# Optimization experiments

Measured on AMD Instinct MI355X. Metric: run time of the kernel, lower is better.

The kernel has to match this reference:

```python
import jax, jax.numpy as jnp
import numpy as np

B, N, IN_DIM, OUT_DIM, C = 8, 8192, 1024, 512, 64
TEMPERATURE = 1.0
LN_EPS = 1e-5


def setup_inputs() -> dict:
    key = jax.random.key(0)
    ks = jax.random.split(key, 6)
    node_embeddings = jax.random.normal(ks[0], (B, N, IN_DIM), dtype=jnp.float32)
    node_mask = jnp.zeros((B, N), dtype=bool)  # True => node is masked out
    # xavier_uniform for cluster_centers [C, OUT_DIM]
    lim_c = float(np.sqrt(6.0 / (C + OUT_DIM)))
    cluster_centers = jax.random.uniform(ks[1], (C, OUT_DIM), jnp.float32, -lim_c, lim_c)
    # nn.Linear default init (kaiming-uniform-ish bounds)
    lim_n = float(1.0 / np.sqrt(IN_DIM))
    W_node = jax.random.uniform(ks[2], (IN_DIM, OUT_DIM), jnp.float32, -lim_n, lim_n)
    b_node = jax.random.uniform(ks[3], (OUT_DIM,), jnp.float32, -lim_n, lim_n)
    lim_k = float(1.0 / np.sqrt(OUT_DIM))
    W_cluster = jax.random.uniform(ks[4], (OUT_DIM, OUT_DIM), jnp.float32, -lim_k, lim_k)
    b_cluster = jax.random.uniform(ks[5], (OUT_DIM,), jnp.float32, -lim_k, lim_k)
    ln_gamma = jnp.ones((OUT_DIM,), jnp.float32)
    ln_beta = jnp.zeros((OUT_DIM,), jnp.float32)
    return {
        "node_embeddings": node_embeddings,
        "node_mask": node_mask,
        "cluster_centers": cluster_centers,
        "W_node": W_node,
        "b_node": b_node,
        "W_cluster": W_cluster,
        "b_cluster": b_cluster,
        "ln_gamma": ln_gamma,
        "ln_beta": ln_beta,
    }


def reference(node_embeddings, node_mask, cluster_centers, W_node, b_node,
              W_cluster, b_cluster, ln_gamma, ln_beta):
    # node projection: [B, N, D]
    node_proj = jnp.einsum('bni,io->bno', node_embeddings, W_node) + b_node
    # projected cluster centers (batch-independent): [C, D]
    ccp = cluster_centers @ W_cluster + b_cluster
    # similarities: [B, C, N]
    sims = jnp.einsum('cd,bnd->bcn', ccp, node_proj) / TEMPERATURE
    sims = jnp.where(node_mask[:, None, :], -jnp.inf, sims)
    assignment_weights = jax.nn.softmax(sims, axis=-1)  # dropout is identity in eval
    # aggregate: [B, C, D], residual add of projected centers
    compressed = jnp.einsum('bcn,bnd->bcd', assignment_weights, node_proj) + ccp
    # LayerNorm over last dim
    mu = jnp.mean(compressed, axis=-1, keepdims=True)
    var = jnp.var(compressed, axis=-1, keepdims=True)
    compressed = (compressed - mu) * jax.lax.rsqrt(var + LN_EPS) * ln_gamma + ln_beta
    return compressed, assignment_weights
```

## Files before the change

### kernel.cpp

```cpp
#include <hip/hip_runtime.h>
#include <hip/hip_bf16.h>
#include <math.h>

#define Bn 8
#define Nn 8192
#define KIN 1024
#define DOUT 512
#define NC 64
#define LN_EPS 1e-5f

typedef short bf16x8 __attribute__((ext_vector_type(8)));
typedef short s8v __attribute__((ext_vector_type(8)));
typedef float f32x4 __attribute__((ext_vector_type(4)));

__device__ __forceinline__ short f2bf(float f) {
    __hip_bfloat16 h = __float2bfloat16(f);
    return __builtin_bit_cast(short, h);
}

__device__ __forceinline__ void load_lds16(const void* g, void* l) {
    __builtin_amdgcn_global_load_lds(
        (const __attribute__((address_space(1))) unsigned int*)g,
        (__attribute__((address_space(3))) unsigned int*)l, 16, 0, 0);
}

__global__ void k_prep_w(const float* __restrict__ W, short* __restrict__ Wt) {
    int o = blockIdx.x * 256 + threadIdx.x;
    int n = o >> 10, k = o & 1023;
    Wt[o] = f2bf(W[k * DOUT + n]);
}

__global__ void k_prep_c(const float* __restrict__ cc, const float* __restrict__ Wc,
                         const float* __restrict__ bc, float* __restrict__ ccp_f,
                         short* __restrict__ ccp_bf) {
    int o = blockIdx.x * 256 + threadIdx.x;
    int c = o >> 9, n = o & 511;
    float a = bc[n];
    for (int k = 0; k < DOUT; ++k) a += cc[c * DOUT + k] * Wc[k * DOUT + n];
    ccp_f[o] = a;
    ccp_bf[o] = f2bf(a);
}

__global__ __launch_bounds__(256) void k_gemm1(
    const float* __restrict__ A, const short* __restrict__ Wt,
    const float* __restrict__ bias, short* __restrict__ proj) {
    __shared__ short As[128 * 40];
    __shared__ short Bs[128 * 32];
    const int tid = threadIdx.x, lane = tid & 63, wv = tid >> 6;
    const int quad = lane >> 4, l15 = lane & 15;
    const int mt = blockIdx.x >> 2, nt = blockIdx.x & 3;
    const int m0 = mt * 128, n0 = nt * 128;
    const int wm = wv >> 1, wn = wv & 1;

    f32x4 acc[4][4];
#pragma unroll
    for (int i = 0; i < 4; ++i)
#pragma unroll
        for (int j = 0; j < 4; ++j) acc[i][j] = (f32x4){0.f, 0.f, 0.f, 0.f};

    const int ar = tid >> 1;
    const int ac = (tid & 1) * 16;
    const float* Ag = A + (size_t)(m0 + ar) * KIN + ac;

    for (int it = 0; it < KIN / 32; ++it) {
        const int k0 = it * 32;
        __syncthreads();
        {
            float4 a0 = *reinterpret_cast<const float4*>(Ag + k0);
            float4 a1 = *reinterpret_cast<const float4*>(Ag + k0 + 4);
            float4 a2 = *reinterpret_cast<const float4*>(Ag + k0 + 8);
            float4 a3 = *reinterpret_cast<const float4*>(Ag + k0 + 12);
            s8v p0, p1;
            p0[0]=f2bf(a0.x); p0[1]=f2bf(a0.y); p0[2]=f2bf(a0.z); p0[3]=f2bf(a0.w);
            p0[4]=f2bf(a1.x); p0[5]=f2bf(a1.y); p0[6]=f2bf(a1.z); p0[7]=f2bf(a1.w);
            p1[0]=f2bf(a2.x); p1[1]=f2bf(a2.y); p1[2]=f2bf(a2.z); p1[3]=f2bf(a2.w);
            p1[4]=f2bf(a3.x); p1[5]=f2bf(a3.y); p1[6]=f2bf(a3.z); p1[7]=f2bf(a3.w);
            *reinterpret_cast<s8v*>(&As[ar * 40 + ac]) = p0;
            *reinterpret_cast<s8v*>(&As[ar * 40 + ac + 8]) = p1;
        }
#pragma unroll
        for (int i = 0; i < 2; ++i) {
            int c = i * 256 + tid;
            int n = c >> 2, kc = c & 3;
            load_lds16(Wt + (size_t)(n0 + n) * KIN + k0 + kc * 8,
                       Bs + (i * 256 + wv * 64) * 8);
        }
        __syncthreads();
        bf16x8 af[4], bfr[4];
#pragma unroll
        for (int mi = 0; mi < 4; ++mi)
            af[mi] = *reinterpret_cast<const bf16x8*>(&As[(wm * 64 + mi * 16 + l15) * 40 + quad * 8]);
#pragma unroll
        for (int ni = 0; ni < 4; ++ni)
            bfr[ni] = *reinterpret_cast<const bf16x8*>(&Bs[(wn * 64 + ni * 16 + l15) * 32 + quad * 8]);
#pragma unroll
        for (int mi = 0; mi < 4; ++mi)
#pragma unroll
            for (int ni = 0; ni < 4; ++ni)
                acc[mi][ni] = __builtin_amdgcn_mfma_f32_16x16x32_bf16(af[mi], bfr[ni], acc[mi][ni], 0, 0, 0);
    }
#pragma unroll
    for (int ni = 0; ni < 4; ++ni) {
        int col = n0 + wn * 64 + ni * 16 + l15;
        float bv = bias[col];
#pragma unroll
        for (int mi = 0; mi < 4; ++mi)
#pragma unroll
            for (int r = 0; r < 4; ++r) {
                int row = m0 + wm * 64 + mi * 16 + quad * 4 + r;
                proj[(size_t)row * DOUT + col] = f2bf(acc[mi][ni][r] + bv);
            }
    }
}

__global__ __launch_bounds__(512) void k_sims(
    const short* __restrict__ ccp_bf, const short* __restrict__ proj,
    float* __restrict__ sims) {
    __shared__ short As[64 * 32];
    __shared__ short Bs[256 * 32];
    const int tid = threadIdx.x, lane = tid & 63, wv = tid >> 6;
    const int quad = lane >> 4, l15 = lane & 15;
    const int b = blockIdx.x >> 5, nt = blockIdx.x & 31;
    const int n0 = nt * 256;
    const int wm = wv & 1, wn = wv >> 1;

    f32x4 acc[2][4];
#pragma unroll
    for (int i = 0; i < 2; ++i)
#pragma unroll
        for (int j = 0; j < 4; ++j) acc[i][j] = (f32x4){0.f, 0.f, 0.f, 0.f};

    for (int it = 0; it < DOUT / 32; ++it) {
        const int k0 = it * 32;
        __syncthreads();
        if (tid < 256) {
            load_lds16(ccp_bf + (size_t)(tid >> 2) * DOUT + k0 + (tid & 3) * 8,
                       As + (wv * 64) * 8);
        }
#pragma unroll
        for (int i = 0; i < 2; ++i) {
            int c = i * 512 + tid;
            int r = c >> 2, kc = c & 3;
            load_lds16(proj + (size_t)(b * Nn + n0 + r) * DOUT + k0 + kc * 8,
                       Bs + (i * 512 + wv * 64) * 8);
        }
        __syncthreads();
        bf16x8 af[2], bfr[4];
#pragma unroll
        for (int mi = 0; mi < 2; ++mi)
            af[mi] = *reinterpret_cast<const bf16x8*>(&As[(wm * 32 + mi * 16 + l15) * 32 + quad * 8]);
#pragma unroll
        for (int ni = 0; ni < 4; ++ni)
            bfr[ni] = *reinterpret_cast<const bf16x8*>(&Bs[(wn * 64 + ni * 16 + l15) * 32 + quad * 8]);
#pragma unroll
        for (int mi = 0; mi < 2; ++mi)
#pragma unroll
            for (int ni = 0; ni < 4; ++ni)
                acc[mi][ni] = __builtin_amdgcn_mfma_f32_16x16x32_bf16(af[mi], bfr[ni], acc[mi][ni], 0, 0, 0);
    }
#pragma unroll
    for (int mi = 0; mi < 2; ++mi)
#pragma unroll
        for (int ni = 0; ni < 4; ++ni)
#pragma unroll
            for (int r = 0; r < 4; ++r) {
                int c = wm * 32 + mi * 16 + quad * 4 + r;
                int n = n0 + wn * 64 + ni * 16 + l15;
                sims[((size_t)b * NC + c) * Nn + n] = acc[mi][ni][r];
            }
}

__global__ __launch_bounds__(256) void k_softmax(
    float* __restrict__ aw, const unsigned char* __restrict__ mask,
    short* __restrict__ aw_bf) {
    __shared__ float red[8];
    const int tid = threadIdx.x, lane = tid & 63, wv = tid >> 6;
    const int b = blockIdx.x >> 6, c = blockIdx.x & 63;
    float* p = aw + ((size_t)b * NC + c) * Nn;
    short* q = aw_bf + ((size_t)b * NC + c) * Nn;
    const unsigned char* mp = mask + b * Nn;

    float v[32];
    float mx = -INFINITY;
#pragma unroll
    for (int i = 0; i < 32; ++i) {
        int idx = tid + i * 256;
        float x = p[idx];
        if (mp[idx]) x = -INFINITY;
        v[i] = x;
        mx = fmaxf(mx, x);
    }
    for (int off = 32; off; off >>= 1) mx = fmaxf(mx, __shfl_xor(mx, off));
    if (lane == 0) red[wv] = mx;
    __syncthreads();
    mx = fmaxf(fmaxf(red[0], red[1]), fmaxf(red[2], red[3]));
    __syncthreads();

    float s = 0.f;
#pragma unroll
    for (int i = 0; i < 32; ++i) {
        v[i] = expf(v[i] - mx);
        s += v[i];
    }
    for (int off = 32; off; off >>= 1) s += __shfl_xor(s, off);
    if (lane == 0) red[wv] = s;
    __syncthreads();
    s = red[0] + red[1] + red[2] + red[3];
    float inv = 1.f / s;
#pragma unroll
    for (int i = 0; i < 32; ++i) {
        int idx = tid + i * 256;
        float w = v[i] * inv;
        p[idx] = w;
        q[idx] = f2bf(w);
    }
}

__global__ __launch_bounds__(256) void k_transpose(
    const short* __restrict__ proj, short* __restrict__ projT) {
    __shared__ short L[64 * 80];
    const int tid = threadIdx.x;
    const int nt = blockIdx.x >> 3, dt = blockIdx.x & 7;
    {
        int n = tid >> 2, d0 = (tid & 3) * 16;
        const short* g = proj + (size_t)(nt * 64 + n) * DOUT + dt * 64 + d0;
        s8v x0 = *reinterpret_cast<const s8v*>(g);
        s8v x1 = *reinterpret_cast<const s8v*>(g + 8);
        *reinterpret_cast<s8v*>(&L[n * 80 + d0]) = x0;
        *reinterpret_cast<s8v*>(&L[n * 80 + d0 + 8]) = x1;
    }
    __syncthreads();
    {
        int d = tid & 63, n0 = (tid >> 6) * 16;
        s8v y0, y1;
#pragma unroll
        for (int j = 0; j < 8; ++j) y0[j] = L[(n0 + j) * 80 + d];
#pragma unroll
        for (int j = 0; j < 8; ++j) y1[j] = L[(n0 + 8 + j) * 80 + d];
        short* o = projT + (size_t)(dt * 64 + d) * (Bn * Nn) + nt * 64 + n0;
        *reinterpret_cast<s8v*>(o) = y0;
        *reinterpret_cast<s8v*>(o + 8) = y1;
    }
}

__global__ __launch_bounds__(256) void k_agg(
    const short* __restrict__ aw_bf, const short* __restrict__ projT,
    float* __restrict__ partial) {
    __shared__ short As[64 * 64];
    __shared__ short Bs[128 * 64];
    const int tid = threadIdx.x, lane = tid & 63, wv = tid >> 6;
    const int quad = lane >> 4, l15 = lane & 15;
    const int b = blockIdx.x >> 6, dt = (blockIdx.x >> 4) & 3, ks = blockIdx.x & 15;
    const int d0 = dt * 128;
    const int wm = wv >> 1, wn = wv & 1;

    f32x4 acc[2][4];
#pragma unroll
    for (int i = 0; i < 2; ++i)
#pragma unroll
        for (int j = 0; j < 4; ++j) acc[i][j] = (f32x4){0.f, 0.f, 0.f, 0.f};

    for (int it = 0; it < 8; ++it) {
        const int nb = ks * 512 + it * 64;
        __syncthreads();
#pragma unroll
        for (int i = 0; i < 2; ++i) {
            int c = i * 256 + tid;
            int r = c >> 3, kc = c & 7;
            load_lds16(aw_bf + ((size_t)b * NC + r) * Nn + nb + kc * 8,
                       As + (i * 256 + wv * 64) * 8);
        }
#pragma unroll
        for (int i = 0; i < 4; ++i) {
            int c = i * 256 + tid;
            int r = c >> 3, kc = c & 7;
            load_lds16(projT + (size_t)(d0 + r) * (Bn * Nn) + b * Nn + nb + kc * 8,
                       Bs + (i * 256 + wv * 64) * 8);
        }
        __syncthreads();
#pragma unroll
        for (int k2 = 0; k2 < 2; ++k2) {
            bf16x8 af[2], bfr[4];
#pragma unroll
            for (int mi = 0; mi < 2; ++mi)
                af[mi] = *reinterpret_cast<const bf16x8*>(&As[(wm * 32 + mi * 16 + l15) * 64 + k2 * 32 + quad * 8]);
#pragma unroll
            for (int ni = 0; ni < 4; ++ni)
                bfr[ni] = *reinterpret_cast<const bf16x8*>(&Bs[(wn * 64 + ni * 16 + l15) * 64 + k2 * 32 + quad * 8]);
#pragma unroll
            for (int mi = 0; mi < 2; ++mi)
#pragma unroll
                for (int ni = 0; ni < 4; ++ni)
                    acc[mi][ni] = __builtin_amdgcn_mfma_f32_16x16x32_bf16(af[mi], bfr[ni], acc[mi][ni], 0, 0, 0);
        }
    }
#pragma unroll
    for (int mi = 0; mi < 2; ++mi)
#pragma unroll
        for (int ni = 0; ni < 4; ++ni)
#pragma unroll
            for (int r = 0; r < 4; ++r) {
                int c = wm * 32 + mi * 16 + quad * 4 + r;
                int d = d0 + wn * 64 + ni * 16 + l15;
                partial[(((size_t)b * 16 + ks) * NC + c) * DOUT + d] = acc[mi][ni][r];
            }
}

__global__ __launch_bounds__(256) void k_ln(
    const float* __restrict__ partial, const float* __restrict__ ccp,
    const float* __restrict__ gamma, const float* __restrict__ beta,
    float* __restrict__ out) {
    __shared__ float red[16];
    const int tid = threadIdx.x, lane = tid & 63, wv = tid >> 6;
    const int b = blockIdx.x >> 6, c = blockIdx.x & 63;
    float v0 = ccp[c * DOUT + tid], v1 = ccp[c * DOUT + tid + 256];
#pragma unroll
    for (int ks = 0; ks < 16; ++ks) {
        const float* pp = partial + (((size_t)b * 16 + ks) * NC + c) * DOUT;
        v0 += pp[tid];
        v1 += pp[tid + 256];
    }
    float s = v0 + v1, sq = v0 * v0 + v1 * v1;
    for (int off = 32; off; off >>= 1) {
        s += __shfl_xor(s, off);
        sq += __shfl_xor(sq, off);
    }
    if (lane == 0) { red[wv] = s; red[8 + wv] = sq; }
    __syncthreads();
    s = red[0] + red[1] + red[2] + red[3];
    sq = red[8] + red[9] + red[10] + red[11];
    float mu = s * (1.f / 512.f);
    float var = sq * (1.f / 512.f) - mu * mu;
    float rs = rsqrtf(var + LN_EPS);
    size_t base = ((size_t)b * NC + c) * DOUT;
    out[base + tid] = (v0 - mu) * rs * gamma[tid] + beta[tid];
    out[base + tid + 256] = (v1 - mu) * rs * gamma[tid + 256] + beta[tid + 256];
}

extern "C" void kernel_launch(void* const* d_in, const int* in_sizes, int n_in,
                              void* d_out, int out_size, void* d_ws, size_t ws_size,
                              hipStream_t stream) {
    const float* node_emb = (const float*)d_in[0];
    const unsigned char* mask = (const unsigned char*)d_in[1];
    const float* cc = (const float*)d_in[2];
    const float* Wn = (const float*)d_in[3];
    const float* bn = (const float*)d_in[4];
    const float* Wc = (const float*)d_in[5];
    const float* bc = (const float*)d_in[6];
    const float* gamma = (const float*)d_in[7];
    const float* beta = (const float*)d_in[8];
    float* out = (float*)d_out;

    char* ws = (char*)d_ws;
    short* proj   = (short*)(ws);
    short* projT  = (short*)(ws + 67108864);
    short* aw_bf  = (short*)(ws + 134217728);
    float* ccp_f  = (float*)(ws + 142606336);
    short* ccp_bf = (short*)(ws + 142737408);
    short* Wt     = (short*)(ws + 142802944);
    float* partial= (float*)(ws + 143851520);

    float* sims = out + (size_t)Bn * NC * DOUT;

    k_prep_w<<<2048, 256, 0, stream>>>(Wn, Wt);
    k_prep_c<<<128, 256, 0, stream>>>(cc, Wc, bc, ccp_f, ccp_bf);
    k_gemm1<<<2048, 256, 0, stream>>>(node_emb, Wt, bn, proj);
    k_sims<<<256, 512, 0, stream>>>(ccp_bf, proj, sims);
    k_softmax<<<512, 256, 0, stream>>>(sims, mask, aw_bf);
    k_transpose<<<8192, 256, 0, stream>>>(proj, projT);
    k_agg<<<512, 256, 0, stream>>>(aw_bf, projT, partial);
    k_ln<<<512, 256, 0, stream>>>(partial, ccp_f, gamma, beta, out);
}
```

Measured before the change: 594.7 us.

## Fuse projT write into GEMM1, retile GEMMs, and speed up prep kernels

The GEMM1 kernel now computes full 64x512 output rows per block and writes both proj and its transpose directly, which removes the separate transpose kernel and its read of proj. The W transpose prep now goes through an LDS tile for coalesced access. The cluster-center prep caches one center row in LDS. The sims and agg kernels are retiled to smaller blocks, and agg uses fewer K-splits, which halves the partial buffer and the work in the LayerNorm reduction. In exchange, the transposed stores from GEMM1 are strided 8-byte writes, and the larger accumulator set adds register pressure.

```diff
diff --git a/kernel.cpp b/kernel.cpp
--- a/kernel.cpp
+++ b/kernel.cpp
@@ -11,6 +11,7 @@
 
 typedef short bf16x8 __attribute__((ext_vector_type(8)));
 typedef short s8v __attribute__((ext_vector_type(8)));
+typedef short s4v __attribute__((ext_vector_type(4)));
 typedef float f32x4 __attribute__((ext_vector_type(4)));
 
 __device__ __forceinline__ short f2bf(float f) {
@@ -24,43 +25,82 @@
         (__attribute__((address_space(3))) unsigned int*)l, 16, 0, 0);
 }
 
-__global__ void k_prep_w(const float* __restrict__ W, short* __restrict__ Wt) {
-    int o = blockIdx.x * 256 + threadIdx.x;
-    int n = o >> 10, k = o & 1023;
-    Wt[o] = f2bf(W[k * DOUT + n]);
-}
-
-__global__ void k_prep_c(const float* __restrict__ cc, const float* __restrict__ Wc,
-                         const float* __restrict__ bc, float* __restrict__ ccp_f,
-                         short* __restrict__ ccp_bf) {
-    int o = blockIdx.x * 256 + threadIdx.x;
-    int c = o >> 9, n = o & 511;
-    float a = bc[n];
-    for (int k = 0; k < DOUT; ++k) a += cc[c * DOUT + k] * Wc[k * DOUT + n];
-    ccp_f[o] = a;
-    ccp_bf[o] = f2bf(a);
-}
-
-__global__ __launch_bounds__(256) void k_gemm1(
+__global__ __launch_bounds__(256) void k_prep_w(const float* __restrict__ W,
+                                                short* __restrict__ Wt) {
+    __shared__ short L[64 * 72];
+    const int tid = threadIdx.x;
+    const int kt = blockIdx.x >> 3, nt = blockIdx.x & 7;
+    const int k0 = kt * 64, n0 = nt * 64;
+    {
+        int r = tid >> 2, c0 = (tid & 3) * 16;
+        const float* g = W + (size_t)(k0 + r) * DOUT + n0 + c0;
+        float4 a0 = *reinterpret_cast<const float4*>(g);
+        float4 a1 = *reinterpret_cast<const float4*>(g + 4);
+        float4 a2 = *reinterpret_cast<const float4*>(g + 8);
+        float4 a3 = *reinterpret_cast<const float4*>(g + 12);
+        s8v p0, p1;
+        p0[0]=f2bf(a0.x); p0[1]=f2bf(a0.y); p0[2]=f2bf(a0.z); p0[3]=f2bf(a0.w);
+        p0[4]=f2bf(a1.x); p0[5]=f2bf(a1.y); p0[6]=f2bf(a1.z); p0[7]=f2bf(a1.w);
+        p1[0]=f2bf(a2.x); p1[1]=f2bf(a2.y); p1[2]=f2bf(a2.z); p1[3]=f2bf(a2.w);
+        p1[4]=f2bf(a3.x); p1[5]=f2bf(a3.y); p1[6]=f2bf(a3.z); p1[7]=f2bf(a3.w);
+        *reinterpret_cast<s8v*>(&L[r * 72 + c0]) = p0;
+        *reinterpret_cast<s8v*>(&L[r * 72 + c0 + 8]) = p1;
+    }
+    __syncthreads();
+    {
+        int n = tid >> 2, kc = (tid & 3) * 16;
+        s8v y0, y1;
+#pragma unroll
+        for (int j = 0; j < 8; ++j) y0[j] = L[(kc + j) * 72 + n];
+#pragma unroll
+        for (int j = 0; j < 8; ++j) y1[j] = L[(kc + 8 + j) * 72 + n];
+        short* o = Wt + (size_t)(n0 + n) * KIN + k0 + kc;
+        *reinterpret_cast<s8v*>(o) = y0;
+        *reinterpret_cast<s8v*>(o + 8) = y1;
+    }
+}
+
+__global__ __launch_bounds__(256) void k_prep_c(
+    const float* __restrict__ cc, const float* __restrict__ Wc,
+    const float* __restrict__ bc, float* __restrict__ ccp_f,
+    short* __restrict__ ccp_bf) {
+    __shared__ float ccs[512];
+    const int tid = threadIdx.x, c = blockIdx.x;
+    ccs[tid] = cc[c * DOUT + tid];
+    ccs[tid + 256] = cc[c * DOUT + tid + 256];
+    __syncthreads();
+    float a0 = bc[tid], a1 = bc[tid + 256];
+    for (int k = 0; k < DOUT; ++k) {
+        float s = ccs[k];
+        a0 += s * Wc[(size_t)k * DOUT + tid];
+        a1 += s * Wc[(size_t)k * DOUT + tid + 256];
+    }
+    ccp_f[c * DOUT + tid] = a0;
+    ccp_f[c * DOUT + tid + 256] = a1;
+    ccp_bf[c * DOUT + tid] = f2bf(a0);
+    ccp_bf[c * DOUT + tid + 256] = f2bf(a1);
+}
+
+__global__ __launch_bounds__(256, 2) void k_gemm1(
     const float* __restrict__ A, const short* __restrict__ Wt,
-    const float* __restrict__ bias, short* __restrict__ proj) {
-    __shared__ short As[128 * 40];
-    __shared__ short Bs[128 * 32];
+    const float* __restrict__ bias, short* __restrict__ proj,
+    short* __restrict__ projT) {
+    __shared__ short As[64 * 40];
+    __shared__ short Bs[512 * 32];
     const int tid = threadIdx.x, lane = tid & 63, wv = tid >> 6;
     const int quad = lane >> 4, l15 = lane & 15;
-    const int mt = blockIdx.x >> 2, nt = blockIdx.x & 3;
-    const int m0 = mt * 128, n0 = nt * 128;
-    const int wm = wv >> 1, wn = wv & 1;
-
-    f32x4 acc[4][4];
+    const int m0 = blockIdx.x * 64;
+
+    f32x4 acc[4][8];
 #pragma unroll
     for (int i = 0; i < 4; ++i)
 #pragma unroll
-        for (int j = 0; j < 4; ++j) acc[i][j] = (f32x4){0.f, 0.f, 0.f, 0.f};
-
-    const int ar = tid >> 1;
-    const int ac = (tid & 1) * 16;
-    const float* Ag = A + (size_t)(m0 + ar) * KIN + ac;
+        for (int j = 0; j < 8; ++j) acc[i][j] = (f32x4){0.f, 0.f, 0.f, 0.f};
+
+    const int ar = tid >> 2;
+    const int ac = (tid & 2) * 8;
+    const int ac2 = (tid & 3) * 8;
+    const float* Ag = A + (size_t)(m0 + ar) * KIN + ac2;
 
     for (int it = 0; it < KIN / 32; ++it) {
         const int k0 = it * 32;
@@ -68,60 +108,60 @@
         {
             float4 a0 = *reinterpret_cast<const float4*>(Ag + k0);
             float4 a1 = *reinterpret_cast<const float4*>(Ag + k0 + 4);
-            float4 a2 = *reinterpret_cast<const float4*>(Ag + k0 + 8);
-            float4 a3 = *reinterpret_cast<const float4*>(Ag + k0 + 12);
-            s8v p0, p1;
-            p0[0]=f2bf(a0.x); p0[1]=f2bf(a0.y); p0[2]=f2bf(a0.z); p0[3]=f2bf(a0.w);
-            p0[4]=f2bf(a1.x); p0[5]=f2bf(a1.y); p0[6]=f2bf(a1.z); p0[7]=f2bf(a1.w);
-            p1[0]=f2bf(a2.x); p1[1]=f2bf(a2.y); p1[2]=f2bf(a2.z); p1[3]=f2bf(a2.w);
-            p1[4]=f2bf(a3.x); p1[5]=f2bf(a3.y); p1[6]=f2bf(a3.z); p1[7]=f2bf(a3.w);
-            *reinterpret_cast<s8v*>(&As[ar * 40 + ac]) = p0;
-            *reinterpret_cast<s8v*>(&As[ar * 40 + ac + 8]) = p1;
-        }
-#pragma unroll
-        for (int i = 0; i < 2; ++i) {
+            s8v p;
+            p[0]=f2bf(a0.x); p[1]=f2bf(a0.y); p[2]=f2bf(a0.z); p[3]=f2bf(a0.w);
+            p[4]=f2bf(a1.x); p[5]=f2bf(a1.y); p[6]=f2bf(a1.z); p[7]=f2bf(a1.w);
+            *reinterpret_cast<s8v*>(&As[ar * 40 + ac2]) = p;
+        }
+#pragma unroll
+        for (int i = 0; i < 8; ++i) {
             int c = i * 256 + tid;
             int n = c >> 2, kc = c & 3;
-            load_lds16(Wt + (size_t)(n0 + n) * KIN + k0 + kc * 8,
+            load_lds16(Wt + (size_t)n * KIN + k0 + kc * 8,
                        Bs + (i * 256 + wv * 64) * 8);
         }
         __syncthreads();
-        bf16x8 af[4], bfr[4];
+        bf16x8 af[4], bfr[8];
 #pragma unroll
         for (int mi = 0; mi < 4; ++mi)
-            af[mi] = *reinterpret_cast<const bf16x8*>(&As[(wm * 64 + mi * 16 + l15) * 40 + quad * 8]);
-#pragma unroll
-        for (int ni = 0; ni < 4; ++ni)
-            bfr[ni] = *reinterpret_cast<const bf16x8*>(&Bs[(wn * 64 + ni * 16 + l15) * 32 + quad * 8]);
+            af[mi] = *reinterpret_cast<const bf16x8*>(&As[(mi * 16 + l15) * 40 + quad * 8]);
+#pragma unroll
+        for (int ni = 0; ni < 8; ++ni)
+            bfr[ni] = *reinterpret_cast<const bf16x8*>(&Bs[(wv * 128 + ni * 16 + l15) * 32 + quad * 8]);
 #pragma unroll
         for (int mi = 0; mi < 4; ++mi)
 #pragma unroll
-            for (int ni = 0; ni < 4; ++ni)
+            for (int ni = 0; ni < 8; ++ni)
                 acc[mi][ni] = __builtin_amdgcn_mfma_f32_16x16x32_bf16(af[mi], bfr[ni], acc[mi][ni], 0, 0, 0);
     }
 #pragma unroll
-    for (int ni = 0; ni < 4; ++ni) {
-        int col = n0 + wn * 64 + ni * 16 + l15;
+    for (int ni = 0; ni < 8; ++ni) {
+        int col = wv * 128 + ni * 16 + l15;
         float bv = bias[col];
 #pragma unroll
-        for (int mi = 0; mi < 4; ++mi)
+        for (int mi = 0; mi < 4; ++mi) {
+            int row0 = m0 + mi * 16 + quad * 4;
+            s4v t;
 #pragma unroll
             for (int r = 0; r < 4; ++r) {
-                int row = m0 + wm * 64 + mi * 16 + quad * 4 + r;
-                proj[(size_t)row * DOUT + col] = f2bf(acc[mi][ni][r] + bv);
+                short v = f2bf(acc[mi][ni][r] + bv);
+                t[r] = v;
+                proj[(size_t)(row0 + r) * DOUT + col] = v;
             }
-    }
-}
-
-__global__ __launch_bounds__(512) void k_sims(
+            *reinterpret_cast<s4v*>(projT + (size_t)col * (Bn * Nn) + row0) = t;
+        }
+    }
+}
+
+__global__ __launch_bounds__(256) void k_sims(
     const short* __restrict__ ccp_bf, const short* __restrict__ proj,
     float* __restrict__ sims) {
     __shared__ short As[64 * 32];
-    __shared__ short Bs[256 * 32];
+    __shared__ short Bs[128 * 32];
     const int tid = threadIdx.x, lane = tid & 63, wv = tid >> 6;
     const int quad = lane >> 4, l15 = lane & 15;
-    const int b = blockIdx.x >> 5, nt = blockIdx.x & 31;
-    const int n0 = nt * 256;
+    const int b = blockIdx.x >> 6, nt = blockIdx.x & 63;
+    const int n0 = nt * 128;
     const int wm = wv & 1, wn = wv >> 1;
 
     f32x4 acc[2][4];
@@ -133,16 +173,21 @@
     for (int it = 0; it < DOUT / 32; ++it) {
         const int k0 = it * 32;
         __syncthreads();
-        if (tid < 256) {
-            load_lds16(ccp_bf + (size_t)(tid >> 2) * DOUT + k0 + (tid & 3) * 8,
-                       As + (wv * 64) * 8);
+        {
+#pragma unroll
+            for (int i = 0; i < 2; ++i) {
+                int c = i * 256 + tid;
+                int r = c >> 2, kc = c & 3;
+                load_lds16(ccp_bf + (size_t)r * DOUT + k0 + kc * 8,
+                           As + (i * 256 + wv * 64) * 8);
+            }
         }
 #pragma unroll
         for (int i = 0; i < 2; ++i) {
-            int c = i * 512 + tid;
+            int c = i * 256 + tid;
             int r = c >> 2, kc = c & 3;
             load_lds16(proj + (size_t)(b * Nn + n0 + r) * DOUT + k0 + kc * 8,
-                       Bs + (i * 512 + wv * 64) * 8);
+                       Bs + (i * 256 + wv * 64) * 8);
         }
         __syncthreads();
         bf16x8 af[2], bfr[4];
@@ -216,43 +261,16 @@
     }
 }
 
-__global__ __launch_bounds__(256) void k_transpose(
-    const short* __restrict__ proj, short* __restrict__ projT) {
-    __shared__ short L[64 * 80];
-    const int tid = threadIdx.x;
-    const int nt = blockIdx.x >> 3, dt = blockIdx.x & 7;
-    {
-        int n = tid >> 2, d0 = (tid & 3) * 16;
-        const short* g = proj + (size_t)(nt * 64 + n) * DOUT + dt * 64 + d0;
-        s8v x0 = *reinterpret_cast<const s8v*>(g);
-        s8v x1 = *reinterpret_cast<const s8v*>(g + 8);
-        *reinterpret_cast<s8v*>(&L[n * 80 + d0]) = x0;
-        *reinterpret_cast<s8v*>(&L[n * 80 + d0 + 8]) = x1;
-    }
-    __syncthreads();
-    {
-        int d = tid & 63, n0 = (tid >> 6) * 16;
-        s8v y0, y1;
-#pragma unroll
-        for (int j = 0; j < 8; ++j) y0[j] = L[(n0 + j) * 80 + d];
-#pragma unroll
-        for (int j = 0; j < 8; ++j) y1[j] = L[(n0 + 8 + j) * 80 + d];
-        short* o = projT + (size_t)(dt * 64 + d) * (Bn * Nn) + nt * 64 + n0;
-        *reinterpret_cast<s8v*>(o) = y0;
-        *reinterpret_cast<s8v*>(o + 8) = y1;
-    }
-}
-
 __global__ __launch_bounds__(256) void k_agg(
     const short* __restrict__ aw_bf, const short* __restrict__ projT,
     float* __restrict__ partial) {
-    __shared__ short As[64 * 64];
-    __shared__ short Bs[128 * 64];
+    __shared__ short As[64 * 32];
+    __shared__ short Bs[128 * 32];
     const int tid = threadIdx.x, lane = tid & 63, wv = tid >> 6;
     const int quad = lane >> 4, l15 = lane & 15;
-    const int b = blockIdx.x >> 6, dt = (blockIdx.x >> 4) & 3, ks = blockIdx.x & 15;
+    const int b = blockIdx.x >> 5, dt = (blockIdx.x >> 3) & 3, ks = blockIdx.x & 7;
     const int d0 = dt * 128;
-    const int wm = wv >> 1, wn = wv & 1;
+    const int wm = wv & 1, wn = wv >> 1;
 
     f32x4 acc[2][4];
 #pragma unroll
@@ -260,39 +278,36 @@
 #pragma unroll
         for (int j = 0; j < 4; ++j) acc[i][j] = (f32x4){0.f, 0.f, 0.f, 0.f};
 
-    for (int it = 0; it < 8; ++it) {
-        const int nb = ks * 512 + it * 64;
+    for (int it = 0; it < 32; ++it) {
+        const int nb = ks * 1024 + it * 32;
         __syncthreads();
 #pragma unroll
         for (int i = 0; i < 2; ++i) {
             int c = i * 256 + tid;
-            int r = c >> 3, kc = c & 7;
+            int r = c >> 2, kc = c & 3;
             load_lds16(aw_bf + ((size_t)b * NC + r) * Nn + nb + kc * 8,
                        As + (i * 256 + wv * 64) * 8);
         }
 #pragma unroll
-        for (int i = 0; i < 4; ++i) {
+        for (int i = 0; i < 2; ++i) {
             int c = i * 256 + tid;
-            int r = c >> 3, kc = c & 7;
+            int r = c >> 2, kc = c & 3;
             load_lds16(projT + (size_t)(d0 + r) * (Bn * Nn) + b * Nn + nb + kc * 8,
                        Bs + (i * 256 + wv * 64) * 8);
         }
         __syncthreads();
-#pragma unroll
-        for (int k2 = 0; k2 < 2; ++k2) {
-            bf16x8 af[2], bfr[4];
-#pragma unroll
-            for (int mi = 0; mi < 2; ++mi)
-                af[mi] = *reinterpret_cast<const bf16x8*>(&As[(wm * 32 + mi * 16 + l15) * 64 + k2 * 32 + quad * 8]);
+        bf16x8 af[2], bfr[4];
+#pragma unroll
+        for (int mi = 0; mi < 2; ++mi)
+            af[mi] = *reinterpret_cast<const bf16x8*>(&As[(wm * 32 + mi * 16 + l15) * 32 + quad * 8]);
+#pragma unroll
+        for (int ni = 0; ni < 4; ++ni)
+            bfr[ni] = *reinterpret_cast<const bf16x8*>(&Bs[(wn * 64 + ni * 16 + l15) * 32 + quad * 8]);
+#pragma unroll
+        for (int mi = 0; mi < 2; ++mi)
 #pragma unroll
             for (int ni = 0; ni < 4; ++ni)
-                bfr[ni] = *reinterpret_cast<const bf16x8*>(&Bs[(wn * 64 + ni * 16 + l15) * 64 + k2 * 32 + quad * 8]);
-#pragma unroll
-            for (int mi = 0; mi < 2; ++mi)
-#pragma unroll
-                for (int ni = 0; ni < 4; ++ni)
-                    acc[mi][ni] = __builtin_amdgcn_mfma_f32_16x16x32_bf16(af[mi], bfr[ni], acc[mi][ni], 0, 0, 0);
-        }
+                acc[mi][ni] = __builtin_amdgcn_mfma_f32_16x16x32_bf16(af[mi], bfr[ni], acc[mi][ni], 0, 0, 0);
     }
 #pragma unroll
     for (int mi = 0; mi < 2; ++mi)
@@ -302,7 +317,7 @@
             for (int r = 0; r < 4; ++r) {
                 int c = wm * 32 + mi * 16 + quad * 4 + r;
                 int d = d0 + wn * 64 + ni * 16 + l15;
-                partial[(((size_t)b * 16 + ks) * NC + c) * DOUT + d] = acc[mi][ni][r];
+                partial[(((size_t)b * 8 + ks) * NC + c) * DOUT + d] = acc[mi][ni][r];
             }
 }
 
@@ -315,8 +330,8 @@
     const int b = blockIdx.x >> 6, c = blockIdx.x & 63;
     float v0 = ccp[c * DOUT + tid], v1 = ccp[c * DOUT + tid + 256];
 #pragma unroll
-    for (int ks = 0; ks < 16; ++ks) {
-        const float* pp = partial + (((size_t)b * 16 + ks) * NC + c) * DOUT;
+    for (int ks = 0; ks < 8; ++ks) {
+        const float* pp = partial + (((size_t)b * 8 + ks) * NC + c) * DOUT;
         v0 += pp[tid];
         v1 += pp[tid + 256];
     }
@@ -362,12 +377,11 @@
 
     float* sims = out + (size_t)Bn * NC * DOUT;
 
-    k_prep_w<<<2048, 256, 0, stream>>>(Wn, Wt);
-    k_prep_c<<<128, 256, 0, stream>>>(cc, Wc, bc, ccp_f, ccp_bf);
-    k_gemm1<<<2048, 256, 0, stream>>>(node_emb, Wt, bn, proj);
-    k_sims<<<256, 512, 0, stream>>>(ccp_bf, proj, sims);
+    k_prep_w<<<128, 256, 0, stream>>>(Wn, Wt);
+    k_prep_c<<<64, 256, 0, stream>>>(cc, Wc, bc, ccp_f, ccp_bf);
+    k_gemm1<<<1024, 256, 0, stream>>>(node_emb, Wt, bn, proj, projT);
+    k_sims<<<512, 256, 0, stream>>>(ccp_bf, proj, sims);
     k_softmax<<<512, 256, 0, stream>>>(sims, mask, aw_bf);
-    k_transpose<<<8192, 256, 0, stream>>>(proj, projT);
-    k_agg<<<512, 256, 0, stream>>>(aw_bf, projT, partial);
+    k_agg<<<256, 256, 0, stream>>>(aw_bf, projT, partial);
     k_ln<<<512, 256, 0, stream>>>(partial, ccp_f, gamma, beta, out);
 }
```

New measurement: 567.8 us. 4.5% less time.
